# Performance work log

Measured on AMD Instinct MI355X. Metric: run time of the kernel, lower is better.

The kernel has to match this reference:

```python
import jax, jax.numpy as jnp
import numpy as np

EPS = 1e-9
ROUTINGS = 3
B, H, CIN, COUT = 16, 8, 32, 32


def setup_inputs() -> dict:
    key = jax.random.key(0)
    k1, k2 = jax.random.split(key)
    # activations/poses from a previous capsule layer are in [0,1) after squashing/sigmoid
    x = jax.random.uniform(k1, (B, H, H, CIN * 17), dtype=jnp.float32)
    w = jax.random.normal(k2, (1, CIN, COUT, 4, 4), dtype=jnp.float32)  # TruncatedNormal(std=1) ~ normal
    beta_v = jnp.zeros((COUT, 18), jnp.float32)
    beta_a = jnp.zeros((COUT,), jnp.float32)
    ij = jnp.stack(jnp.meshgrid(jnp.arange(H), jnp.arange(H), indexing='ij'), axis=-1)
    coord_add = ij.reshape(H * H, 2).astype(jnp.float32) / H  # [H*H, 2] scaled coords
    return {"x": x, "w": w, "beta_v": beta_v, "beta_a": beta_a, "coord_add": coord_add}


def em_routing(votes, activation, beta_v, beta_a, routings):
    # votes: [N, ci, co, ch=18], activation: [N, ci, 1]
    N, ci, co, ch = votes.shape
    r = jnp.full((N, ci, co), 1.0 / co, dtype=votes.dtype)
    miu = sigma_sq = act_out = None
    for it in range(routings):  # small fixed routing count
        if it > 0:
            # E-step: Gaussian log-likelihood of each vote under each output capsule
            log_p = -0.5 * jnp.log(sigma_sq) - jnp.square(votes - miu) / (2.0 * sigma_sq)  # [N,ci,co,ch]
            log_p = log_p - (jnp.max(log_p, axis=(2, 3), keepdims=True) - jnp.log(10.0))
            p = jnp.exp(jnp.sum(log_p, axis=3))  # [N,ci,co]
            ap = p * act_out.reshape(N, 1, co)
            r = ap / (jnp.sum(ap, axis=2, keepdims=True) + EPS)
        # M-step
        r = r * activation  # weight by input activation, broadcast over co
        r = r / (jnp.sum(r, axis=2, keepdims=True) + EPS)
        r_sum = jnp.sum(r, axis=1, keepdims=True)  # [N,1,co]
        r1 = (r / (r_sum + EPS))[..., None]        # [N,ci,co,1]
        miu = jnp.sum(votes * r1, axis=1, keepdims=True)                        # [N,1,co,ch]
        sigma_sq = jnp.sum(jnp.square(votes - miu) * r1, axis=1, keepdims=True) + EPS
        if it == routings - 1:
            rs = r_sum.reshape(N, co, 1)
            cost_h = (beta_v + 0.5 * jnp.log(sigma_sq.reshape(N, co, ch))) * rs  # [N,co,ch]
            ac_lambda = 0.01 * (it + 1)
            act_out = jax.nn.softmax(ac_lambda * (beta_a - jnp.sum(cost_h, axis=2)), axis=-1)
        else:
            act_out = jax.nn.softmax(r_sum.reshape(N, co), axis=-1)
    return miu, act_out


def reference(x, w, beta_v, beta_a, coord_add):
    Bx, Hx, Wx, C = x.shape
    ci = C // 17
    xr = x.reshape(Bx, Hx, Wx, ci, 17)
    pose = xr[..., :16].reshape(-1, ci, 16)   # [N, ci, 16], N = B*H*W
    act = xr[..., 16].reshape(-1, ci, 1)      # [N, ci, 1]
    N = pose.shape[0]
    co = w.shape[2]
    # mat_transform: batched 4x4 matmul pose @ w per (input capsule, output capsule)
    votes = jnp.einsum('niab,icbd->nicad', pose.reshape(N, ci, 4, 4), w[0]).reshape(N, ci, co, 16)
    # coordinate addition: 2 extra channels with spatial coords, tiled over batch/capsules
    coord = jnp.broadcast_to(coord_add.reshape(Hx * Wx, 1, 1, 2), (Hx * Wx, ci, co, 2))
    coord = jnp.tile(coord, (Bx, 1, 1, 1))    # [N, ci, co, 2]
    votes = jnp.concatenate([coord, votes], axis=3)  # [N, ci, co, 18]
    miu, act_out = em_routing(votes, act, beta_v, beta_a, ROUTINGS)
    # global average pool over the spatial grid
    outputs = jnp.mean(act_out.reshape(Bx, Hx, Wx, co), axis=(1, 2))                       # [B, co]
    pose_out = jnp.mean(miu.reshape(Bx, Hx, Wx, co * 18), axis=(1, 2)).reshape(Bx, co, 18)  # [B, co, 18]
    return outputs, pose_out
```

## Files before the change

kernel.cpp:

```cpp
#include <hip/hip_runtime.h>
#include <math.h>


#define CI 32
#define CO 32
#define CH 18
#define NPOS 1024
#define PSTR 38
#define OUT_ACT (16 * CO)

constexpr float EPSF = 1e-9f;
constexpr float LN10 = 2.302585092994046f;

__device__ __forceinline__ float fast_rcp(float x) {
    return __builtin_amdgcn_rcpf(x);
}

template <int CTRL>
__device__ __forceinline__ float dppf(float x) {
    union { float f; int i; } u; u.f = x;
    u.i = __builtin_amdgcn_update_dpp(u.i, u.i, CTRL, 0xF, 0xF, true);
    return u.f;
}

__device__ __forceinline__ float bf_sum32(float x) {
    x += dppf<0xB1>(x);
    x += dppf<0x4E>(x);
    x += dppf<0x141>(x);
    x += dppf<0x140>(x);
    x += __shfl_xor(x, 16);
    return x;
}
__device__ __forceinline__ float bf_max32(float x) {
    x = fmaxf(x, dppf<0xB1>(x));
    x = fmaxf(x, dppf<0x4E>(x));
    x = fmaxf(x, dppf<0x141>(x));
    x = fmaxf(x, dppf<0x140>(x));
    x = fmaxf(x, __shfl_xor(x, 16));
    return x;
}

__global__ __launch_bounds__(256) void caps_em_kernel(
    const float* __restrict__ x,
    const float* __restrict__ w,
    const float* __restrict__ beta_v,
    const float* __restrict__ beta_a,
    const float* __restrict__ coord_add,
    float* __restrict__ out)
{
    const int n  = blockIdx.x;
    const int t  = threadIdx.x;
    const int c  = t & 31;
    const int ig = t >> 5;
    const int wv = t >> 6;

    __shared__ float pose[CI][16];
    __shared__ float act_in[CI];
    __shared__ float part[4][CO * PSTR];
    __shared__ float2 muq_s[CO * 19];
    __shared__ float base_s[CO * 19];

    const float* xrow = x + n * (CI * 17);
    for (int e = t; e < CI * 17; e += 256) {
        int i = e / 17, k = e % 17;
        float val = xrow[e];
        if (k < 16) pose[i][k] = val;
        else        act_in[i]  = val;
    }
    const float cx = coord_add[(n & 63) * 2 + 0];
    const float cy = coord_add[(n & 63) * 2 + 1];
    __syncthreads();

    float v[4][16];
    float a_in[4];
    #pragma unroll
    for (int k = 0; k < 4; ++k) {
        int i = ig * 4 + k;
        a_in[k] = act_in[i];
        float pr[16], wr[16];
        const float4* pp4 = (const float4*)pose[i];
        const float4* wp4 = (const float4*)(w + ((i * CO + c) << 4));
        #pragma unroll
        for (int q = 0; q < 4; ++q) {
            float4 pf = pp4[q];
            pr[q*4+0] = pf.x; pr[q*4+1] = pf.y; pr[q*4+2] = pf.z; pr[q*4+3] = pf.w;
            float4 wf = wp4[q];
            wr[q*4+0] = wf.x; wr[q*4+1] = wf.y; wr[q*4+2] = wf.z; wr[q*4+3] = wf.w;
        }
        #pragma unroll
        for (int a = 0; a < 4; ++a) {
            #pragma unroll
            for (int d = 0; d < 4; ++d) {
                float s = pr[a*4+0] * wr[0*4+d];
                s += pr[a*4+1] * wr[1*4+d];
                s += pr[a*4+2] * wr[2*4+d];
                s += pr[a*4+3] * wr[3*4+d];
                v[k][a*4+d] = s;
            }
        }
    }

    float rr[4];
    float act_c = 0.0f;

    for (int it = 0; it < 3; ++it) {
        if (it > 0) {
            float S[4]  = {0.0f, 0.0f, 0.0f, 0.0f};
            float mx[4] = {-3.0e38f, -3.0e38f, -3.0e38f, -3.0e38f};
            const float2* muqc = &muq_s[c * 19];
            const float*  bsc  = &base_s[c * 19];
            #pragma unroll
            for (int ch = 0; ch < CH; ++ch) {
                float2 mq = muqc[ch];
                float  bs = bsc[ch];
                #pragma unroll
                for (int k = 0; k < 4; ++k) {
                    float vv = (ch == 0) ? cx : ((ch == 1) ? cy : v[k][ch - 2]);
                    float d  = vv - mq.x;
                    float lp = bs - d * d * mq.y;
                    S[k] += lp;
                    mx[k] = fmaxf(mx[k], lp);
                }
            }
            #pragma unroll
            for (int k = 0; k < 4; ++k) {
                float m = bf_max32(mx[k]);
                float shift = 18.0f * (m - LN10);
                float p  = __expf(S[k] - shift);
                float ap = p * act_c;
                float A  = bf_sum32(ap);
                float invA = fast_rcp(A + EPSF);
                float re = ap * invA;
                float sk = A * invA;
                float an = a_in[k];
                rr[k] = re * an * fast_rcp(an * sk + EPSF);
            }
        } else {
            #pragma unroll
            for (int k = 0; k < 4; ++k) {
                float an = a_in[k];
                rr[k] = (1.0f / 32.0f) * an * fast_rcp(an + EPSF);
            }
        }

        {
            float* pp = &part[wv][c * PSTR];
            float prr = rr[0] + rr[1] + rr[2] + rr[3];
            float prs = prr + __shfl_xor(prr, 32);
            pp[0] = prs;
            float s0 = cx * prr, s1v = cy * prr;
            s0  += __shfl_xor(s0, 32);
            s1v += __shfl_xor(s1v, 32);
            pp[1] = s0;  pp[19] = cx * s0;
            pp[2] = s1v; pp[20] = cy * s1v;
            #pragma unroll
            for (int ch = 2; ch < CH; ++ch) {
                float s = 0.0f, s2 = 0.0f;
                #pragma unroll
                for (int k = 0; k < 4; ++k) {
                    float rv = rr[k] * v[k][ch - 2];
                    s  += rv;
                    s2 += rv * v[k][ch - 2];
                }
                s  += __shfl_xor(s, 32);
                s2 += __shfl_xor(s2, 32);
                pp[1 + ch]  = s;
                pp[19 + ch] = s2;
            }
        }
        __syncthreads();

        float r_sum;
        {
            const int base = c * PSTR;
            float rs = part[0][base] + part[1][base] + part[2][base] + part[3][base];
            r_sum = rs;
            float rsinv = fast_rcp(rs + EPSF);
            float s1 = rs * rsinv;
            float c2 = 2.0f - s1;
            for (int ch = ig; ch < CH; ch += 8) {
                int jm = base + 1 + ch, jv = base + 19 + ch;
                float mu_un = part[0][jm] + part[1][jm] + part[2][jm] + part[3][jm];
                float v2_un = part[0][jv] + part[1][jv] + part[2][jv] + part[3][jv];
                float mu  = mu_un * rsinv;
                float sig = fmaxf(v2_un * rsinv - mu * mu * c2, 0.0f) + EPSF;
                muq_s[c * 19 + ch]  = make_float2(mu, 0.5f * fast_rcp(sig));
                base_s[c * 19 + ch] = -0.5f * __logf(sig);
            }
        }
        __syncthreads();

        float logit;
        if (it == 2) {
            float cost = 0.0f;
            #pragma unroll
            for (int ch = 0; ch < CH; ++ch)
                cost += beta_v[c * CH + ch] - base_s[c * 19 + ch];
            logit = 0.03f * (beta_a[c] - cost * r_sum);
        } else {
            logit = r_sum;
        }
        float mxl = bf_max32(logit);
        float ex  = __expf(logit - mxl);
        act_c = ex * fast_rcp(bf_sum32(ex));
    }

    const float inv64 = 1.0f / 64.0f;
    const int b = n >> 6;
    if (t < CO) atomicAdd(&out[b * CO + t], act_c * inv64);
    for (int e = t; e < CO * CH; e += 256) {
        int cc = e / CH, ch = e - cc * CH;
        atomicAdd(&out[OUT_ACT + b * (CO * CH) + e], muq_s[cc * 19 + ch].x * inv64);
    }
}

extern "C" void kernel_launch(void* const* d_in, const int* in_sizes, int n_in,
                              void* d_out, int out_size, void* d_ws, size_t ws_size,
                              hipStream_t stream) {
    const float* x         = (const float*)d_in[0];
    const float* w         = (const float*)d_in[1];
    const float* beta_v    = (const float*)d_in[2];
    const float* beta_a    = (const float*)d_in[3];
    const float* coord_add = (const float*)d_in[4];
    float* out = (float*)d_out;

    hipMemsetAsync(out, 0, (size_t)out_size * sizeof(float), stream);
    caps_em_kernel<<<dim3(NPOS), dim3(256), 0, stream>>>(
        x, w, beta_v, beta_a, coord_add, out);
}
```

Measured before the change: 90.46 us.

## Process two spatial positions per block to reuse weight loads and halve atomics

Each block now handles two positions instead of one. The weight row is loaded once and applied to both poses, and the two positions' mean and activation are summed before the atomicAdd, which halves the atomic traffic. The per-warp partial sums move to a float2-packed layout and launch bounds request two blocks per CU. In exchange, register and LDS use per block roughly double, which may lower occupancy or cause register spills, and only half as many blocks are launched.

Result: faster. 84.18 us (-6.9%).

```diff
diff --git a/kernel.cpp b/kernel.cpp
--- a/kernel.cpp
+++ b/kernel.cpp
@@ -6,8 +6,7 @@
 #define CO 32
 #define CH 18
 #define NPOS 1024
-#define PSTR 38
-#define OUT_ACT (16 * CO)
+#define OUT_ACT (16 * 32)
 
 constexpr float EPSF = 1e-9f;
 constexpr float LN10 = 2.302585092994046f;
@@ -40,7 +39,7 @@
     return x;
 }
 
-__global__ __launch_bounds__(256) void caps_em_kernel(
+__global__ __launch_bounds__(256, 2) void caps_em_kernel(
     const float* __restrict__ x,
     const float* __restrict__ w,
     const float* __restrict__ beta_v,
@@ -48,169 +47,200 @@
     const float* __restrict__ coord_add,
     float* __restrict__ out)
 {
-    const int n  = blockIdx.x;
+    const int n0 = blockIdx.x * 2;
     const int t  = threadIdx.x;
     const int c  = t & 31;
     const int ig = t >> 5;
     const int wv = t >> 6;
 
-    __shared__ float pose[CI][16];
-    __shared__ float act_in[CI];
-    __shared__ float part[4][CO * PSTR];
-    __shared__ float2 muq_s[CO * 19];
-    __shared__ float base_s[CO * 19];
-
-    const float* xrow = x + n * (CI * 17);
-    for (int e = t; e < CI * 17; e += 256) {
-        int i = e / 17, k = e % 17;
+    __shared__ float  pose[2][CI][16];
+    __shared__ float  act_in[2][CI];
+    __shared__ float  rs_part[2][4][CO];
+    __shared__ float2 part2[2][4][CO * 19];
+    __shared__ float2 muq_s[2][CO * 19];
+    __shared__ float  base_s[2][CO * 19];
+
+    const float* xrow = x + n0 * (CI * 17);
+    for (int e = t; e < 2 * CI * 17; e += 256) {
+        int p = e >= CI * 17;
+        int idx = e - p * (CI * 17);
+        int i = idx / 17, k = idx % 17;
         float val = xrow[e];
-        if (k < 16) pose[i][k] = val;
-        else        act_in[i]  = val;
-    }
-    const float cx = coord_add[(n & 63) * 2 + 0];
-    const float cy = coord_add[(n & 63) * 2 + 1];
+        if (k < 16) pose[p][i][k] = val;
+        else        act_in[p][i]  = val;
+    }
+    float cxy[2][2];
+    #pragma unroll
+    for (int p = 0; p < 2; ++p) {
+        cxy[p][0] = coord_add[((n0 + p) & 63) * 2 + 0];
+        cxy[p][1] = coord_add[((n0 + p) & 63) * 2 + 1];
+    }
     __syncthreads();
 
-    float v[4][16];
-    float a_in[4];
+    float v[2][4][16];
     #pragma unroll
     for (int k = 0; k < 4; ++k) {
         int i = ig * 4 + k;
-        a_in[k] = act_in[i];
-        float pr[16], wr[16];
-        const float4* pp4 = (const float4*)pose[i];
+        float wr[16];
         const float4* wp4 = (const float4*)(w + ((i * CO + c) << 4));
         #pragma unroll
         for (int q = 0; q < 4; ++q) {
-            float4 pf = pp4[q];
-            pr[q*4+0] = pf.x; pr[q*4+1] = pf.y; pr[q*4+2] = pf.z; pr[q*4+3] = pf.w;
             float4 wf = wp4[q];
             wr[q*4+0] = wf.x; wr[q*4+1] = wf.y; wr[q*4+2] = wf.z; wr[q*4+3] = wf.w;
         }
         #pragma unroll
-        for (int a = 0; a < 4; ++a) {
-            #pragma unroll
-            for (int d = 0; d < 4; ++d) {
-                float s = pr[a*4+0] * wr[0*4+d];
-                s += pr[a*4+1] * wr[1*4+d];
-                s += pr[a*4+2] * wr[2*4+d];
-                s += pr[a*4+3] * wr[3*4+d];
-                v[k][a*4+d] = s;
-            }
-        }
-    }
-
-    float rr[4];
-    float act_c = 0.0f;
+        for (int p = 0; p < 2; ++p) {
+            float pr[16];
+            const float4* pp4 = (const float4*)pose[p][i];
+            #pragma unroll
+            for (int q = 0; q < 4; ++q) {
+                float4 pf = pp4[q];
+                pr[q*4+0] = pf.x; pr[q*4+1] = pf.y; pr[q*4+2] = pf.z; pr[q*4+3] = pf.w;
+            }
+            #pragma unroll
+            for (int a = 0; a < 4; ++a) {
+                #pragma unroll
+                for (int d = 0; d < 4; ++d) {
+                    float s = pr[a*4+0] * wr[0*4+d];
+                    s += pr[a*4+1] * wr[1*4+d];
+                    s += pr[a*4+2] * wr[2*4+d];
+                    s += pr[a*4+3] * wr[3*4+d];
+                    v[p][k][a*4+d] = s;
+                }
+            }
+        }
+    }
+
+    float rr[2][4];
+    float act_c[2] = {0.0f, 0.0f};
+    float r_sum[2];
 
     for (int it = 0; it < 3; ++it) {
         if (it > 0) {
-            float S[4]  = {0.0f, 0.0f, 0.0f, 0.0f};
-            float mx[4] = {-3.0e38f, -3.0e38f, -3.0e38f, -3.0e38f};
-            const float2* muqc = &muq_s[c * 19];
-            const float*  bsc  = &base_s[c * 19];
+            float S[2][4], mx[2][4];
+            #pragma unroll
+            for (int p = 0; p < 2; ++p)
+                #pragma unroll
+                for (int k = 0; k < 4; ++k) { S[p][k] = 0.0f; mx[p][k] = -3.0e38f; }
             #pragma unroll
             for (int ch = 0; ch < CH; ++ch) {
-                float2 mq = muqc[ch];
-                float  bs = bsc[ch];
+                #pragma unroll
+                for (int p = 0; p < 2; ++p) {
+                    float2 mq = muq_s[p][c * 19 + ch];
+                    float  bs = base_s[p][c * 19 + ch];
+                    #pragma unroll
+                    for (int k = 0; k < 4; ++k) {
+                        float vv = (ch == 0) ? cxy[p][0]
+                                 : ((ch == 1) ? cxy[p][1] : v[p][k][ch - 2]);
+                        float d  = vv - mq.x;
+                        float lp = bs - d * d * mq.y;
+                        S[p][k] += lp;
+                        mx[p][k] = fmaxf(mx[p][k], lp);
+                    }
+                }
+            }
+            #pragma unroll
+            for (int k = 0; k < 4; ++k) {
+                #pragma unroll
+                for (int p = 0; p < 2; ++p) {
+                    float m = bf_max32(mx[p][k]);
+                    float shift = 18.0f * (m - LN10);
+                    float pe = __expf(S[p][k] - shift);
+                    float ap = pe * act_c[p];
+                    float A  = bf_sum32(ap);
+                    float invA = fast_rcp(A + EPSF);
+                    float re = ap * invA;
+                    float sk = A * invA;
+                    float an = act_in[p][ig * 4 + k];
+                    rr[p][k] = re * an * fast_rcp(an * sk + EPSF);
+                }
+            }
+        } else {
+            #pragma unroll
+            for (int p = 0; p < 2; ++p)
                 #pragma unroll
                 for (int k = 0; k < 4; ++k) {
-                    float vv = (ch == 0) ? cx : ((ch == 1) ? cy : v[k][ch - 2]);
-                    float d  = vv - mq.x;
-                    float lp = bs - d * d * mq.y;
-                    S[k] += lp;
-                    mx[k] = fmaxf(mx[k], lp);
-                }
-            }
-            #pragma unroll
-            for (int k = 0; k < 4; ++k) {
-                float m = bf_max32(mx[k]);
-                float shift = 18.0f * (m - LN10);
-                float p  = __expf(S[k] - shift);
-                float ap = p * act_c;
-                float A  = bf_sum32(ap);
-                float invA = fast_rcp(A + EPSF);
-                float re = ap * invA;
-                float sk = A * invA;
-                float an = a_in[k];
-                rr[k] = re * an * fast_rcp(an * sk + EPSF);
-            }
-        } else {
-            #pragma unroll
-            for (int k = 0; k < 4; ++k) {
-                float an = a_in[k];
-                rr[k] = (1.0f / 32.0f) * an * fast_rcp(an + EPSF);
-            }
-        }
-
-        {
-            float* pp = &part[wv][c * PSTR];
-            float prr = rr[0] + rr[1] + rr[2] + rr[3];
+                    float an = act_in[p][ig * 4 + k];
+                    rr[p][k] = (1.0f / 32.0f) * an * fast_rcp(an + EPSF);
+                }
+        }
+
+        #pragma unroll
+        for (int p = 0; p < 2; ++p) {
+            float prr = rr[p][0] + rr[p][1] + rr[p][2] + rr[p][3];
             float prs = prr + __shfl_xor(prr, 32);
-            pp[0] = prs;
-            float s0 = cx * prr, s1v = cy * prr;
-            s0  += __shfl_xor(s0, 32);
-            s1v += __shfl_xor(s1v, 32);
-            pp[1] = s0;  pp[19] = cx * s0;
-            pp[2] = s1v; pp[20] = cy * s1v;
+            rs_part[p][wv][c] = prs;
+            float2* pp = &part2[p][wv][c * 19];
+            float cx = cxy[p][0], cy = cxy[p][1];
+            float s0 = cx * prr, s1 = cy * prr;
+            s0 += __shfl_xor(s0, 32);
+            s1 += __shfl_xor(s1, 32);
+            pp[0] = make_float2(s0, cx * s0);
+            pp[1] = make_float2(s1, cy * s1);
             #pragma unroll
             for (int ch = 2; ch < CH; ++ch) {
                 float s = 0.0f, s2 = 0.0f;
                 #pragma unroll
                 for (int k = 0; k < 4; ++k) {
-                    float rv = rr[k] * v[k][ch - 2];
+                    float rv = rr[p][k] * v[p][k][ch - 2];
                     s  += rv;
-                    s2 += rv * v[k][ch - 2];
+                    s2 += rv * v[p][k][ch - 2];
                 }
                 s  += __shfl_xor(s, 32);
                 s2 += __shfl_xor(s2, 32);
-                pp[1 + ch]  = s;
-                pp[19 + ch] = s2;
+                pp[ch] = make_float2(s, s2);
             }
         }
         __syncthreads();
 
-        float r_sum;
-        {
-            const int base = c * PSTR;
-            float rs = part[0][base] + part[1][base] + part[2][base] + part[3][base];
-            r_sum = rs;
+        #pragma unroll
+        for (int p = 0; p < 2; ++p) {
+            float rs = rs_part[p][0][c] + rs_part[p][1][c]
+                     + rs_part[p][2][c] + rs_part[p][3][c];
+            r_sum[p] = rs;
             float rsinv = fast_rcp(rs + EPSF);
             float s1 = rs * rsinv;
             float c2 = 2.0f - s1;
             for (int ch = ig; ch < CH; ch += 8) {
-                int jm = base + 1 + ch, jv = base + 19 + ch;
-                float mu_un = part[0][jm] + part[1][jm] + part[2][jm] + part[3][jm];
-                float v2_un = part[0][jv] + part[1][jv] + part[2][jv] + part[3][jv];
+                int j = c * 19 + ch;
+                float2 a0 = part2[p][0][j], a1 = part2[p][1][j];
+                float2 a2 = part2[p][2][j], a3 = part2[p][3][j];
+                float mu_un = a0.x + a1.x + a2.x + a3.x;
+                float v2_un = a0.y + a1.y + a2.y + a3.y;
                 float mu  = mu_un * rsinv;
                 float sig = fmaxf(v2_un * rsinv - mu * mu * c2, 0.0f) + EPSF;
-                muq_s[c * 19 + ch]  = make_float2(mu, 0.5f * fast_rcp(sig));
-                base_s[c * 19 + ch] = -0.5f * __logf(sig);
+                muq_s[p][j]  = make_float2(mu, 0.5f * fast_rcp(sig));
+                base_s[p][j] = -0.5f * __logf(sig);
             }
         }
         __syncthreads();
 
-        float logit;
-        if (it == 2) {
-            float cost = 0.0f;
-            #pragma unroll
-            for (int ch = 0; ch < CH; ++ch)
-                cost += beta_v[c * CH + ch] - base_s[c * 19 + ch];
-            logit = 0.03f * (beta_a[c] - cost * r_sum);
-        } else {
-            logit = r_sum;
-        }
-        float mxl = bf_max32(logit);
-        float ex  = __expf(logit - mxl);
-        act_c = ex * fast_rcp(bf_sum32(ex));
+        #pragma unroll
+        for (int p = 0; p < 2; ++p) {
+            float logit;
+            if (it == 2) {
+                float cost = 0.0f;
+                #pragma unroll
+                for (int ch = 0; ch < CH; ++ch)
+                    cost += beta_v[c * CH + ch] - base_s[p][c * 19 + ch];
+                logit = 0.03f * (beta_a[c] - cost * r_sum[p]);
+            } else {
+                logit = r_sum[p];
+            }
+            float mxl = bf_max32(logit);
+            float ex  = __expf(logit - mxl);
+            act_c[p] = ex * fast_rcp(bf_sum32(ex));
+        }
     }
 
     const float inv64 = 1.0f / 64.0f;
-    const int b = n >> 6;
-    if (t < CO) atomicAdd(&out[b * CO + t], act_c * inv64);
+    const int b = n0 >> 6;
+    if (t < CO)
+        atomicAdd(&out[b * CO + t], (act_c[0] + act_c[1]) * inv64);
     for (int e = t; e < CO * CH; e += 256) {
         int cc = e / CH, ch = e - cc * CH;
-        atomicAdd(&out[OUT_ACT + b * (CO * CH) + e], muq_s[cc * 19 + ch].x * inv64);
+        float s = muq_s[0][cc * 19 + ch].x + muq_s[1][cc * 19 + ch].x;
+        atomicAdd(&out[OUT_ACT + b * (CO * CH) + e], s * inv64);
     }
 }
 
@@ -225,6 +255,6 @@
     float* out = (float*)d_out;
 
     hipMemsetAsync(out, 0, (size_t)out_size * sizeof(float), stream);
-    caps_em_kernel<<<dim3(NPOS), dim3(256), 0, stream>>>(
+    caps_em_kernel<<<dim3(NPOS / 2), dim3(256), 0, stream>>>(
         x, w, beta_v, beta_a, coord_add, out);
 }
```
